# Optimization experiments

Measured on AMD Instinct MI355X. Metric: run time of the kernel, lower is better.

## Reference

```python
import jax, jax.numpy as jnp
import numpy as np

ALPHA = 0.1  # LeakyReLU negative slope
F_OUT = 128

def _leaky(x):
    return jnp.where(x >= 0, x, ALPHA * x)

def setup_inputs() -> dict:
    key = jax.random.key(0)
    ks = jax.random.split(key, 12)
    B, N, F_IN = 4, 4096, 128
    q = jax.random.normal(ks[0], (B, N, F_IN), jnp.float32)
    k = jax.random.normal(ks[1], (B, N, F_IN), jnp.float32)
    v = jax.random.normal(ks[2], (B, N, F_IN), jnp.float32)
    adj = jax.random.randint(ks[3], (B, N, N), 0, 2, jnp.int32)
    s = 1.0 / np.sqrt(F_IN)
    Wq_w = jax.random.uniform(ks[4], (F_OUT, F_IN), jnp.float32, -s, s)
    Wq_b = jax.random.uniform(ks[5], (F_OUT,), jnp.float32, -s, s)
    Wk_w = jax.random.uniform(ks[6], (F_OUT, F_IN), jnp.float32, -s, s)
    Wk_b = jax.random.uniform(ks[7], (F_OUT,), jnp.float32, -s, s)
    Wv_w = jax.random.uniform(ks[8], (F_OUT, F_IN), jnp.float32, -s, s)
    Wv_b = jax.random.uniform(ks[9], (F_OUT,), jnp.float32, -s, s)
    # xavier_uniform with gain=1.414 on (2F,1)
    lim = 1.414 * np.sqrt(6.0 / (2 * F_OUT + 1))
    a = jax.random.uniform(ks[10], (2 * F_OUT, 1), jnp.float32, -lim, lim)
    so = 1.0 / np.sqrt(F_OUT)
    Wo_w = jax.random.uniform(ks[11], (F_OUT, F_OUT), jnp.float32, -so, so)
    return {"q": q, "k": k, "v": v, "adj": adj, "Wq_w": Wq_w, "Wq_b": Wq_b,
            "Wk_w": Wk_w, "Wk_b": Wk_b, "Wv_w": Wv_w, "Wv_b": Wv_b,
            "a": a, "Wo_w": Wo_w}

def reference(q, k, v, adj, Wq_w, Wq_b, Wk_w, Wk_b, Wv_w, Wv_b, a, Wo_w):
    qp = q @ Wq_w.T + Wq_b                      # (B,N,F)
    kp = k @ Wk_w.T + Wk_b
    vp = v @ Wv_w.T + Wv_b
    Wh1 = qp @ a[:F_OUT]                        # (B,N,1)
    Wh2 = kp @ a[F_OUT:]                        # (B,N,1)
    e = _leaky(Wh1 + jnp.swapaxes(Wh2, 1, 2))   # (B,N,N)
    e = jnp.where(adj > 0, e, jnp.float32(-1e9))
    att = jax.nn.softmax(e, axis=-1)
    h = jnp.einsum('bnm,bmf->bnf', att, vp)     # (B,N,F)
    return _leaky(h @ Wo_w.T)
```

## Files before the change

### kernel.cpp

```cpp
#include <hip/hip_runtime.h>


constexpr int B = 4, N = 4096, F = 128;
constexpr int BN = B * N;
constexpr int BK = 64;
constexpr int SPLITS = 4;
constexpr int JC = N / SPLITS;
constexpr int NIT = JC / BK;
#define ALPHA 0.1f

using float4v = __attribute__((ext_vector_type(4))) float;
using short8 = __attribute__((ext_vector_type(8))) short;

__device__ __forceinline__ float leaky(float x) { return x >= 0.f ? x : ALPHA * x; }
__device__ __forceinline__ unsigned short f2bf(float x) {
    unsigned u = __float_as_uint(x);
    u = (u + 0x7FFFu + ((u >> 16) & 1u)) >> 16;
    return (unsigned short)u;
}
__device__ __forceinline__ unsigned pack_bf2(float lo, float hi) {
    unsigned a = __float_as_uint(lo), b2 = __float_as_uint(hi);
    a = a + 0x7FFFu + ((a >> 16) & 1u);
    b2 = b2 + 0x7FFFu + ((b2 >> 16) & 1u);
    return __builtin_amdgcn_perm(b2, a, 0x07060302u);
}

__global__ void k_prep(const float* __restrict__ Wq_w, const float* __restrict__ Wq_b,
                       const float* __restrict__ Wk_w, const float* __restrict__ Wk_b,
                       const float* __restrict__ a, float* __restrict__ c1,
                       float* __restrict__ c2, float* __restrict__ d12) {
    __shared__ float as[2 * F];
    __shared__ float red[2 * F];
    int t = threadIdx.x;
    as[t] = a[t];
    __syncthreads();
    int f = t & 127;
    const float* W = (t < F) ? Wq_w : Wk_w;
    const float* ao = (t < F) ? as : as + F;
    float s = 0.f;
#pragma unroll 8
    for (int o = 0; o < F; o++) s = fmaf(W[o * F + f], ao[o], s);
    if (t < F) c1[f] = s; else c2[f] = s;
    red[t] = (t < F) ? Wq_b[f] * as[f] : Wk_b[f] * as[F + f];
    __syncthreads();
    for (int st = 64; st > 0; st >>= 1) {
        if (f < st) red[t] += red[t + st];
        __syncthreads();
    }
    if (t == 0) d12[0] = red[0];
    if (t == F) d12[1] = red[F];
}

__global__ void k_wh(const float* __restrict__ q, const float* __restrict__ k,
                     const float* __restrict__ c1, const float* __restrict__ c2,
                     const float* __restrict__ d12,
                     float* __restrict__ Wh1, float* __restrict__ Wh2) {
    __shared__ float c1s[F], c2s[F];
    int t = threadIdx.x;
    if (t < F) c1s[t] = c1[t]; else c2s[t - F] = c2[t - F];
    __syncthreads();
    int row = blockIdx.x * 8 + (t >> 5);
    int lane = t & 31;
    float4 q4 = reinterpret_cast<const float4*>(q)[row * 32 + lane];
    float4 k4 = reinterpret_cast<const float4*>(k)[row * 32 + lane];
    float s1 = q4.x * c1s[lane * 4 + 0] + q4.y * c1s[lane * 4 + 1] +
               q4.z * c1s[lane * 4 + 2] + q4.w * c1s[lane * 4 + 3];
    float s2 = k4.x * c2s[lane * 4 + 0] + k4.y * c2s[lane * 4 + 1] +
               k4.z * c2s[lane * 4 + 2] + k4.w * c2s[lane * 4 + 3];
    for (int m = 16; m > 0; m >>= 1) { s1 += __shfl_xor(s1, m); s2 += __shfl_xor(s2, m); }
    if (lane == 0) { Wh1[row] = s1 + d12[0]; Wh2[row] = s2 + d12[1]; }
}

__global__ void k_max2(const float* __restrict__ Wh2, float* __restrict__ M2) {
    int b = blockIdx.x, t = threadIdx.x;
    float m = -1e30f;
    for (int i = t; i < N; i += 256) m = fmaxf(m, Wh2[b * N + i]);
    __shared__ float red[256];
    red[t] = m;
    __syncthreads();
    for (int s = 128; s > 0; s >>= 1) { if (t < s) red[t] = fmaxf(red[t], red[t + s]); __syncthreads(); }
    if (t == 0) M2[b] = red[0];
}

__global__ void k_tab(const float* __restrict__ Wh1, const float* __restrict__ Wh2,
                      const float* __restrict__ M2,
                      float* __restrict__ P1, float* __restrict__ Q1,
                      float* __restrict__ P2, float* __restrict__ Q2) {
    int i = blockIdx.x * 256 + threadIdx.x;
    int b = i >> 12;
    float w1 = Wh1[i], w2 = Wh2[i];
    float mi = leaky(w1 + M2[b]);
    P1[i] = __expf(w1 - mi);
    Q1[i] = __expf(ALPHA * w1 - mi);
    P2[i] = __expf(w2);
    Q2[i] = __expf(ALPHA * w2);
}

__global__ __launch_bounds__(256) void k_vp(const float* __restrict__ v,
                                            const float* __restrict__ Wv_w,
                                            const float* __restrict__ Wv_b,
                                            unsigned short* __restrict__ vpT) {
    __shared__ float vs[32][F];
    __shared__ float Ws[F][129];
    __shared__ unsigned short ts[F][40];
    int t = threadIdx.x;
    int row0g = blockIdx.x * 32;
    int b = row0g >> 12;
    int row0 = row0g & (N - 1);
    {
        const float4* src = reinterpret_cast<const float4*>(v + row0g * F);
        float4* dst = reinterpret_cast<float4*>(&vs[0][0]);
#pragma unroll
        for (int u = 0; u < 4; u++) dst[u * 256 + t] = src[u * 256 + t];
    }
    {
        const float4* src = reinterpret_cast<const float4*>(Wv_w);
#pragma unroll
        for (int u = 0; u < 16; u++) {
            int unit = u * 256 + t;
            int r = unit >> 5, s = unit & 31;
            float4 val = src[unit];
            Ws[r][s * 4 + 0] = val.x; Ws[r][s * 4 + 1] = val.y;
            Ws[r][s * 4 + 2] = val.z; Ws[r][s * 4 + 3] = val.w;
        }
    }
    int f = t & 127, g = t >> 7;
    float bias = Wv_b[f];
    __syncthreads();
    float acc[16];
#pragma unroll
    for (int r = 0; r < 16; r++) acc[r] = bias;
    for (int kk = 0; kk < F; kk++) {
        float wk = Ws[f][kk];
#pragma unroll
        for (int r = 0; r < 16; r++) acc[r] = fmaf(vs[g * 16 + r][kk], wk, acc[r]);
    }
#pragma unroll
    for (int r = 0; r < 16; r++) ts[f][g * 16 + r] = f2bf(acc[r]);
    __syncthreads();
    int fr = t >> 1, hseg = t & 1;
    uint4 d0 = *reinterpret_cast<uint4*>(&ts[fr][hseg * 16]);
    uint4 d1 = *reinterpret_cast<uint4*>(&ts[fr][hseg * 16 + 8]);
    unsigned short* dst = vpT + ((size_t)(b * F + fr) * N + row0 + hseg * 16);
    *reinterpret_cast<uint4*>(dst) = d0;
    *reinterpret_cast<uint4*>(dst + 8) = d1;
}

__global__ __launch_bounds__(256, 4) void k_attn(
    const unsigned short* __restrict__ vpT, const int* __restrict__ adj,
    const float* __restrict__ Wh1, const float* __restrict__ P1, const float* __restrict__ Q1,
    const float* __restrict__ P2, const float* __restrict__ Q2, const float* __restrict__ Wh2,
    float* __restrict__ h_part, float* __restrict__ den_part) {
    __shared__ __align__(16) float sP2[JC], sQ2[JC], sW2[JC];
    int t = threadIdx.x;
    int idx = blockIdx.x;
    int split = idx & 3;
    int tile = (idx >> 2) & 63;
    int b = idx >> 8;
    int i0 = tile * 64;
    int jb0 = split * JC;
    int widx = t >> 6, lane = t & 63, m = lane & 15, q = lane >> 4;

    {
        reinterpret_cast<float4*>(sP2)[t] = reinterpret_cast<const float4*>(P2 + b * N + jb0)[t];
        reinterpret_cast<float4*>(sQ2)[t] = reinterpret_cast<const float4*>(Q2 + b * N + jb0)[t];
        reinterpret_cast<float4*>(sW2)[t] = reinterpret_cast<const float4*>(Wh2 + b * N + jb0)[t];
    }

    int gi = b * N + i0 + widx * 16 + m;
    float p1 = P1[gi], q1 = Q1[gi], t1 = -Wh1[gi];

    const unsigned short* vbl = vpT + (size_t)b * F * N + (size_t)m * N + jb0 + q * 8;
    const int* adjr = adj + (size_t)gi * N + jb0 + q * 8;

    __syncthreads();

    int4 aregA[4], aregB[4];

    auto load_adj = [&](int it, int4* ar) {
#pragma unroll
        for (int kh = 0; kh < 2; kh++) {
            const int* p = adjr + it * BK + kh * 32;
            ar[kh * 2 + 0] = *reinterpret_cast<const int4*>(p);
            ar[kh * 2 + 1] = *reinterpret_cast<const int4*>(p + 4);
        }
    };

    float4v acc[8];
#pragma unroll
    for (int nt = 0; nt < 8; nt++) acc[nt] = (float4v){0.f, 0.f, 0.f, 0.f};
    float den = 0.f;

    auto gen_af = [&](const int4& a0, const int4& a1, const float4& x2a, const float4& x2b,
                      const float4& p2a, const float4& p2b, const float4& q2a,
                      const float4& q2b, float& dn) -> short8 {
        float w0 = a0.x ? ((x2a.x >= t1) ? p1 * p2a.x : q1 * q2a.x) : 0.f;
        float w1 = a0.y ? ((x2a.y >= t1) ? p1 * p2a.y : q1 * q2a.y) : 0.f;
        float w2 = a0.z ? ((x2a.z >= t1) ? p1 * p2a.z : q1 * q2a.z) : 0.f;
        float w3 = a0.w ? ((x2a.w >= t1) ? p1 * p2a.w : q1 * q2a.w) : 0.f;
        float w4 = a1.x ? ((x2b.x >= t1) ? p1 * p2b.x : q1 * q2b.x) : 0.f;
        float w5 = a1.y ? ((x2b.y >= t1) ? p1 * p2b.y : q1 * q2b.y) : 0.f;
        float w6 = a1.z ? ((x2b.z >= t1) ? p1 * p2b.z : q1 * q2b.z) : 0.f;
        float w7 = a1.w ? ((x2b.w >= t1) ? p1 * p2b.w : q1 * q2b.w) : 0.f;
        dn += ((w0 + w1) + (w2 + w3)) + ((w4 + w5) + (w6 + w7));
        union { short8 s; uint4 u; } r;
        r.u.x = pack_bf2(w0, w1); r.u.y = pack_bf2(w2, w3);
        r.u.z = pack_bf2(w4, w5); r.u.w = pack_bf2(w6, w7);
        return r.s;
    };

    auto body = [&](int it, int4* cur, int4* nxt) {
        if (it + 1 < NIT) load_adj(it + 1, nxt);
#pragma unroll
        for (int kh = 0; kh < 2; kh++) {
            int jl = it * BK + kh * 32 + q * 8;
            float4 x2a = *reinterpret_cast<const float4*>(&sW2[jl]);
            float4 x2b = *reinterpret_cast<const float4*>(&sW2[jl + 4]);
            float4 p2a = *reinterpret_cast<const float4*>(&sP2[jl]);
            float4 p2b = *reinterpret_cast<const float4*>(&sP2[jl + 4]);
            float4 q2a = *reinterpret_cast<const float4*>(&sQ2[jl]);
            float4 q2b = *reinterpret_cast<const float4*>(&sQ2[jl + 4]);
            short8 af = gen_af(cur[kh * 2 + 0], cur[kh * 2 + 1], x2a, x2b,
                               p2a, p2b, q2a, q2b, den);
            const unsigned short* vk = vbl + it * BK + kh * 32;
#pragma unroll
            for (int nt = 0; nt < 8; nt++) {
                short8 bf = *reinterpret_cast<const short8*>(vk + (size_t)nt * 16 * N);
                acc[nt] = __builtin_amdgcn_mfma_f32_16x16x32_bf16(af, bf, acc[nt], 0, 0, 0);
            }
        }
    };

    load_adj(0, aregA);
#pragma unroll 1
    for (int ith = 0; ith < NIT / 2; ith++) {
        body(ith * 2 + 0, aregA, aregB);
        body(ith * 2 + 1, aregB, aregA);
    }

    den += __shfl_xor(den, 16);
    den += __shfl_xor(den, 32);
    float* dp = den_part + (size_t)split * BN;
    if (q == 0) dp[gi] = den;
    float* hp = h_part + (size_t)split * BN * F;
    int orow = b * N + i0 + widx * 16 + q * 4;
#pragma unroll
    for (int nt = 0; nt < 8; nt++)
#pragma unroll
        for (int r = 0; r < 4; r++)
            hp[(size_t)(orow + r) * F + nt * 16 + m] = acc[nt][r];
}

__global__ __launch_bounds__(256) void k_out(const float* __restrict__ h_part,
                                             const float* __restrict__ den_part,
                                             const float* __restrict__ Wo_w,
                                             float* __restrict__ out) {
    __shared__ float hs[32][F];
    __shared__ float Ws[F][129];
    int t = threadIdx.x;
    int row0 = blockIdx.x * 32;
    {
        const float4* src = reinterpret_cast<const float4*>(Wo_w);
#pragma unroll
        for (int u = 0; u < 16; u++) {
            int unit = u * 256 + t;
            int r = unit >> 5, s = unit & 31;
            float4 val = src[unit];
            Ws[r][s * 4 + 0] = val.x; Ws[r][s * 4 + 1] = val.y;
            Ws[r][s * 4 + 2] = val.z; Ws[r][s * 4 + 3] = val.w;
        }
    }
#pragma unroll
    for (int u = 0; u < 4; u++) {
        int unit = u * 256 + t;
        int r = unit >> 5, s = unit & 31;
        size_t off = (size_t)(row0 + r) * F + s * 4;
        float4 h0 = *reinterpret_cast<const float4*>(h_part + off);
        float4 h1 = *reinterpret_cast<const float4*>(h_part + (size_t)BN * F + off);
        float4 h2 = *reinterpret_cast<const float4*>(h_part + (size_t)2 * BN * F + off);
        float4 h3 = *reinterpret_cast<const float4*>(h_part + (size_t)3 * BN * F + off);
        float dsum = den_part[row0 + r] + den_part[BN + row0 + r] +
                     den_part[2 * BN + row0 + r] + den_part[3 * BN + row0 + r];
        float inv = 1.f / dsum;
        hs[r][s * 4 + 0] = (h0.x + h1.x + h2.x + h3.x) * inv;
        hs[r][s * 4 + 1] = (h0.y + h1.y + h2.y + h3.y) * inv;
        hs[r][s * 4 + 2] = (h0.z + h1.z + h2.z + h3.z) * inv;
        hs[r][s * 4 + 3] = (h0.w + h1.w + h2.w + h3.w) * inv;
    }
    __syncthreads();
    int f = t & 127, g = t >> 7;
    float acc[16];
#pragma unroll
    for (int r = 0; r < 16; r++) acc[r] = 0.f;
    for (int kk = 0; kk < F; kk++) {
        float wk = Ws[f][kk];
#pragma unroll
        for (int r = 0; r < 16; r++) acc[r] = fmaf(hs[g * 16 + r][kk], wk, acc[r]);
    }
#pragma unroll
    for (int r = 0; r < 16; r++) out[(size_t)(row0 + g * 16 + r) * F + f] = leaky(acc[r]);
}

extern "C" void kernel_launch(void* const* d_in, const int* in_sizes, int n_in,
                              void* d_out, int out_size, void* d_ws, size_t ws_size,
                              hipStream_t stream) {
    const float* q    = (const float*)d_in[0];
    const float* k    = (const float*)d_in[1];
    const float* v    = (const float*)d_in[2];
    const int*   adj  = (const int*)d_in[3];
    const float* Wq_w = (const float*)d_in[4];
    const float* Wq_b = (const float*)d_in[5];
    const float* Wk_w = (const float*)d_in[6];
    const float* Wk_b = (const float*)d_in[7];
    const float* Wv_w = (const float*)d_in[8];
    const float* Wv_b = (const float*)d_in[9];
    const float* a    = (const float*)d_in[10];
    const float* Wo_w = (const float*)d_in[11];
    float* out = (float*)d_out;
    float* ws = (float*)d_ws;

    unsigned short* vpT = (unsigned short*)ws;
    float* h_part   = ws + BN * F / 2;
    float* den_part = h_part + (size_t)SPLITS * BN * F;
    float* Wh1 = den_part + SPLITS * BN;
    float* Wh2 = Wh1 + BN;
    float* P1  = Wh2 + BN;
    float* Q1  = P1 + BN;
    float* P2  = Q1 + BN;
    float* Q2  = P2 + BN;
    float* c1  = Q2 + BN;
    float* c2  = c1 + F;
    float* d12 = c2 + F;
    float* M2  = d12 + 2;

    k_prep<<<1, 256, 0, stream>>>(Wq_w, Wq_b, Wk_w, Wk_b, a, c1, c2, d12);
    k_wh<<<BN / 8, 256, 0, stream>>>(q, k, c1, c2, d12, Wh1, Wh2);
    k_max2<<<B, 256, 0, stream>>>(Wh2, M2);
    k_tab<<<BN / 256, 256, 0, stream>>>(Wh1, Wh2, M2, P1, Q1, P2, Q2);
    k_vp<<<BN / 32, 256, 0, stream>>>(v, Wv_w, Wv_b, vpT);
    k_attn<<<B * 64 * SPLITS, 256, 0, stream>>>(vpT, adj, Wh1, P1, Q1, P2, Q2, Wh2,
                                                h_part, den_part);
    k_out<<<BN / 32, 256, 0, stream>>>(h_part, den_part, Wo_w, out);
}
```

Before: 632.6 us.

## Bit-pack adjacency in a pre-pass and stage V tiles through LDS double buffer

Adds a k_pack kernel that compresses the int32 adjacency matrix into 64-bit ballot masks. The attention kernel then reads one mask word per 64 columns instead of int4 loads, and decodes the mask bits when building the A fragments. The V tiles are now loaded cooperatively into a double-buffered shared-memory array instead of being read per wave straight from global memory. This cuts global traffic inside k_attn, but the pre-pass still has to read the full adjacency once, and it adds a barrier per iteration, more LDS use and a lower occupancy bound.

```diff
diff --git a/kernel.cpp b/kernel.cpp
--- a/kernel.cpp
+++ b/kernel.cpp
@@ -11,6 +11,7 @@
 
 using float4v = __attribute__((ext_vector_type(4))) float;
 using short8 = __attribute__((ext_vector_type(8))) short;
+typedef unsigned long long ull;
 
 __device__ __forceinline__ float leaky(float x) { return x >= 0.f ? x : ALPHA * x; }
 __device__ __forceinline__ unsigned short f2bf(float x) {
@@ -23,6 +24,26 @@
     a = a + 0x7FFFu + ((a >> 16) & 1u);
     b2 = b2 + 0x7FFFu + ((b2 >> 16) & 1u);
     return __builtin_amdgcn_perm(b2, a, 0x07060302u);
+}
+
+__global__ __launch_bounds__(256) void k_pack(const int* __restrict__ adj,
+                                              ull* __restrict__ pack) {
+    const long long GROUPS = (long long)B * N * N / 256;
+    int t = threadIdx.x;
+    int lane = t & 63;
+    long long gw = ((long long)blockIdx.x * 256 + t) >> 6;
+    long long nw = ((long long)gridDim.x * 256) >> 6;
+    for (long long g = gw; g < GROUPS; g += nw) {
+        long long base = g * 256;
+        ull m0 = __ballot(adj[base + lane] != 0);
+        ull m1 = __ballot(adj[base + 64 + lane] != 0);
+        ull m2 = __ballot(adj[base + 128 + lane] != 0);
+        ull m3 = __ballot(adj[base + 192 + lane] != 0);
+        if (lane < 4) {
+            ull w = (lane == 0) ? m0 : (lane == 1) ? m1 : (lane == 2) ? m2 : m3;
+            pack[g * 4 + lane] = w;
+        }
+    }
 }
 
 __global__ void k_prep(const float* __restrict__ Wq_w, const float* __restrict__ Wq_b,
@@ -146,11 +167,12 @@
     *reinterpret_cast<uint4*>(dst + 8) = d1;
 }
 
-__global__ __launch_bounds__(256, 4) void k_attn(
-    const unsigned short* __restrict__ vpT, const int* __restrict__ adj,
+__global__ __launch_bounds__(256, 3) void k_attn(
+    const unsigned short* __restrict__ vpT, const ull* __restrict__ pack,
     const float* __restrict__ Wh1, const float* __restrict__ P1, const float* __restrict__ Q1,
     const float* __restrict__ P2, const float* __restrict__ Q2, const float* __restrict__ Wh2,
     float* __restrict__ h_part, float* __restrict__ den_part) {
+    __shared__ __align__(16) unsigned short bs[2][F][72];
     __shared__ __align__(16) float sP2[JC], sQ2[JC], sW2[JC];
     int t = threadIdx.x;
     int idx = blockIdx.x;
@@ -169,20 +191,24 @@
 
     int gi = b * N + i0 + widx * 16 + m;
     float p1 = P1[gi], q1 = Q1[gi], t1 = -Wh1[gi];
-
-    const unsigned short* vbl = vpT + (size_t)b * F * N + (size_t)m * N + jb0 + q * 8;
-    const int* adjr = adj + (size_t)gi * N + jb0 + q * 8;
-
-    __syncthreads();
-
-    int4 aregA[4], aregB[4];
-
-    auto load_adj = [&](int it, int4* ar) {
-#pragma unroll
-        for (int kh = 0; kh < 2; kh++) {
-            const int* p = adjr + it * BK + kh * 32;
-            ar[kh * 2 + 0] = *reinterpret_cast<const int4*>(p);
-            ar[kh * 2 + 1] = *reinterpret_cast<const int4*>(p + 4);
+    const ull* pk = pack + (size_t)gi * (N / 64) + jb0 / 64;
+    const unsigned short* vb = vpT + (size_t)b * F * N + jb0;
+
+    uint4 sreg[4];
+    auto load_stage = [&](int it) {
+#pragma unroll
+        for (int u = 0; u < 4; u++) {
+            int unit = u * 256 + t;
+            int r = unit >> 3, s = unit & 7;
+            sreg[u] = *reinterpret_cast<const uint4*>(vb + (size_t)r * N + it * BK + s * 8);
+        }
+    };
+    auto write_stage = [&](int pb) {
+#pragma unroll
+        for (int u = 0; u < 4; u++) {
+            int unit = u * 256 + t;
+            int r = unit >> 3, s = unit & 7;
+            *reinterpret_cast<uint4*>(&bs[pb][r][s * 8]) = sreg[u];
         }
     };
 
@@ -191,17 +217,17 @@
     for (int nt = 0; nt < 8; nt++) acc[nt] = (float4v){0.f, 0.f, 0.f, 0.f};
     float den = 0.f;
 
-    auto gen_af = [&](const int4& a0, const int4& a1, const float4& x2a, const float4& x2b,
+    auto gen_af = [&](unsigned bt, const float4& x2a, const float4& x2b,
                       const float4& p2a, const float4& p2b, const float4& q2a,
                       const float4& q2b, float& dn) -> short8 {
-        float w0 = a0.x ? ((x2a.x >= t1) ? p1 * p2a.x : q1 * q2a.x) : 0.f;
-        float w1 = a0.y ? ((x2a.y >= t1) ? p1 * p2a.y : q1 * q2a.y) : 0.f;
-        float w2 = a0.z ? ((x2a.z >= t1) ? p1 * p2a.z : q1 * q2a.z) : 0.f;
-        float w3 = a0.w ? ((x2a.w >= t1) ? p1 * p2a.w : q1 * q2a.w) : 0.f;
-        float w4 = a1.x ? ((x2b.x >= t1) ? p1 * p2b.x : q1 * q2b.x) : 0.f;
-        float w5 = a1.y ? ((x2b.y >= t1) ? p1 * p2b.y : q1 * q2b.y) : 0.f;
-        float w6 = a1.z ? ((x2b.z >= t1) ? p1 * p2b.z : q1 * q2b.z) : 0.f;
-        float w7 = a1.w ? ((x2b.w >= t1) ? p1 * p2b.w : q1 * q2b.w) : 0.f;
+        float w0 = (bt & 1u)   ? ((x2a.x >= t1) ? p1 * p2a.x : q1 * q2a.x) : 0.f;
+        float w1 = (bt & 2u)   ? ((x2a.y >= t1) ? p1 * p2a.y : q1 * q2a.y) : 0.f;
+        float w2 = (bt & 4u)   ? ((x2a.z >= t1) ? p1 * p2a.z : q1 * q2a.z) : 0.f;
+        float w3 = (bt & 8u)   ? ((x2a.w >= t1) ? p1 * p2a.w : q1 * q2a.w) : 0.f;
+        float w4 = (bt & 16u)  ? ((x2b.x >= t1) ? p1 * p2b.x : q1 * q2b.x) : 0.f;
+        float w5 = (bt & 32u)  ? ((x2b.y >= t1) ? p1 * p2b.y : q1 * q2b.y) : 0.f;
+        float w6 = (bt & 64u)  ? ((x2b.z >= t1) ? p1 * p2b.z : q1 * q2b.z) : 0.f;
+        float w7 = (bt & 128u) ? ((x2b.w >= t1) ? p1 * p2b.w : q1 * q2b.w) : 0.f;
         dn += ((w0 + w1) + (w2 + w3)) + ((w4 + w5) + (w6 + w7));
         union { short8 s; uint4 u; } r;
         r.u.x = pack_bf2(w0, w1); r.u.y = pack_bf2(w2, w3);
@@ -209,8 +235,11 @@
         return r.s;
     };
 
-    auto body = [&](int it, int4* cur, int4* nxt) {
-        if (it + 1 < NIT) load_adj(it + 1, nxt);
+    auto body = [&](int it, int pb, ull pw, ull& pwn) {
+        if (it + 1 < NIT) {
+            load_stage(it + 1);
+            pwn = pk[it + 1];
+        }
 #pragma unroll
         for (int kh = 0; kh < 2; kh++) {
             int jl = it * BK + kh * 32 + q * 8;
@@ -220,22 +249,28 @@
             float4 p2b = *reinterpret_cast<const float4*>(&sP2[jl + 4]);
             float4 q2a = *reinterpret_cast<const float4*>(&sQ2[jl]);
             float4 q2b = *reinterpret_cast<const float4*>(&sQ2[jl + 4]);
-            short8 af = gen_af(cur[kh * 2 + 0], cur[kh * 2 + 1], x2a, x2b,
-                               p2a, p2b, q2a, q2b, den);
-            const unsigned short* vk = vbl + it * BK + kh * 32;
+            unsigned bt = ((unsigned)(pw >> (kh * 32)) >> (q * 8)) & 0xFFu;
+            short8 af = gen_af(bt, x2a, x2b, p2a, p2b, q2a, q2b, den);
 #pragma unroll
             for (int nt = 0; nt < 8; nt++) {
-                short8 bf = *reinterpret_cast<const short8*>(vk + (size_t)nt * 16 * N);
+                short8 bf = *reinterpret_cast<const short8*>(&bs[pb][nt * 16 + m][kh * 32 + q * 8]);
                 acc[nt] = __builtin_amdgcn_mfma_f32_16x16x32_bf16(af, bf, acc[nt], 0, 0, 0);
             }
         }
+        if (it + 1 < NIT) write_stage(pb ^ 1);
+        __syncthreads();
     };
 
-    load_adj(0, aregA);
+    ull pwA, pwB;
+    load_stage(0);
+    pwA = pk[0];
+    write_stage(0);
+    __syncthreads();
+
 #pragma unroll 1
     for (int ith = 0; ith < NIT / 2; ith++) {
-        body(ith * 2 + 0, aregA, aregB);
-        body(ith * 2 + 1, aregB, aregA);
+        body(ith * 2 + 0, 0, pwA, pwB);
+        body(ith * 2 + 1, 1, pwB, pwA);
     }
 
     den += __shfl_xor(den, 16);
@@ -332,13 +367,17 @@
     float* c2  = c1 + F;
     float* d12 = c2 + F;
     float* M2  = d12 + 2;
-
+    size_t off = (size_t)((M2 + B) - ws);
+    off = (off + 1) & ~(size_t)1;
+    ull* pack = (ull*)(ws + off);
+
+    k_pack<<<2048, 256, 0, stream>>>(adj, pack);
     k_prep<<<1, 256, 0, stream>>>(Wq_w, Wq_b, Wk_w, Wk_b, a, c1, c2, d12);
     k_wh<<<BN / 8, 256, 0, stream>>>(q, k, c1, c2, d12, Wh1, Wh2);
     k_max2<<<B, 256, 0, stream>>>(Wh2, M2);
     k_tab<<<BN / 256, 256, 0, stream>>>(Wh1, Wh2, M2, P1, Q1, P2, Q2);
     k_vp<<<BN / 32, 256, 0, stream>>>(v, Wv_w, Wv_b, vpT);
-    k_attn<<<B * 64 * SPLITS, 256, 0, stream>>>(vpT, adj, Wh1, P1, Q1, P2, Q2, Wh2,
+    k_attn<<<B * 64 * SPLITS, 256, 0, stream>>>(vpT, pack, Wh1, P1, Q1, P2, Q2, Wh2,
                                                 h_part, den_part);
     k_out<<<BN / 32, 256, 0, stream>>>(h_part, den_part, Wo_w, out);
 }
```

Result: faster. 538.7 us (-14.8%).
